# Kernel optimization log

Hardware: AMD Instinct MI355X
Metric: run time of the kernel (lower is better)

Reference implementation:

```python
import jax, jax.numpy as jnp
import numpy as np

B, C, H, W = 4, 256, 64, 64
C8 = C // 8


def setup_inputs() -> dict:
    key = jax.random.key(0)
    k1, k2, k3, k4 = jax.random.split(key, 4)
    x = jax.random.normal(k1, (B, C, H, W), dtype=jnp.float32)
    # conv1d(ks=1, bias=False) projections -> plain [out, in] matrices
    Wq = jax.random.normal(k2, (C8, C), dtype=jnp.float32) * (1.0 / np.sqrt(C))
    Wk = jax.random.normal(k3, (C8, C), dtype=jnp.float32) * (1.0 / np.sqrt(C))
    Wv = jax.random.normal(k4, (C, C), dtype=jnp.float32) * (1.0 / np.sqrt(C))
    gamma = jnp.zeros((1,), dtype=jnp.float32)
    return {"x": x, "Wq": Wq, "Wk": Wk, "Wv": Wv, "gamma": gamma}


def reference(x, Wq, Wk, Wv, gamma):
    b, c, h, w = x.shape
    xf = x.reshape(b, c, h * w)                      # [B, C, N]
    f = jnp.einsum('oc,bcn->bon', Wq, xf)            # [B, C/8, N] query
    g = jnp.einsum('oc,bcn->bon', Wk, xf)            # [B, C/8, N] key
    hv = jnp.einsum('oc,bcn->bon', Wv, xf)           # [B, C,   N] value
    # scores[b,i,j] = sum_c f[b,c,i] * g[b,c,j]; softmax over dim=1 (i)
    scores = jnp.einsum('bci,bcj->bij', f, g)        # [B, N, N]
    beta = jax.nn.softmax(scores, axis=1)
    # o[b,c,j] = sum_i hv[b,c,i] * beta[b,i,j]
    o = jnp.einsum('bci,bij->bcj', hv, beta)         # [B, C, N]
    out = gamma[0] * o + xf
    return out.reshape(b, c, h, w)
```

## Files before the change

### kernel.cpp

```cpp
#include <hip/hip_runtime.h>

#define B_  4
#define C_  256
#define C8_ 32
#define N_  4096
#define HVS_ (N_ + 64)

#define TJ 128
#define KI 64
#define SPLITS 4

typedef __attribute__((ext_vector_type(8)))  short bf16x8;
typedef __attribute__((ext_vector_type(16))) float f32x16;

union FragAB { bf16x8 v; unsigned short u[8]; };

__device__ __forceinline__ unsigned short f2bf(float x) {
    unsigned u = __float_as_uint(x);
    unsigned r = u + 0x7FFFu + ((u >> 16) & 1u);
    return (unsigned short)(r >> 16);
}
__device__ __forceinline__ unsigned pack2bf(float a, float b) {
    return (unsigned)f2bf(a) | ((unsigned)f2bf(b) << 16);
}
__device__ __forceinline__ unsigned cvtpk(float lo, float hi) {
    unsigned r;
    asm("v_cvt_pk_bf16_f32 %0, %1, %2" : "=v"(r) : "v"(lo), "v"(hi));
    return r;
}

__global__ __launch_bounds__(256) void prep_w_kernel(
    const float* __restrict__ Wq, const float* __restrict__ Wk,
    const float* __restrict__ Wv, unsigned short* __restrict__ Wbf)
{
    int idx = (blockIdx.x * 256 + threadIdx.x) * 4;
    int row = idx >> 8;
    int col = idx & 255;
    const float* src; int r;
    if (row < 32)      { src = Wq; r = row;      }
    else if (row < 64) { src = Wk; r = row - 32; }
    else               { src = Wv; r = row - 64; }
    float4 v = *(const float4*)&src[r * 256 + col];
    uint2 o; o.x = pack2bf(v.x, v.y); o.y = pack2bf(v.z, v.w);
    *(uint2*)&Wbf[idx] = o;
}

__global__ __launch_bounds__(256) void prep_x_kernel(
    const float* __restrict__ x, unsigned short* __restrict__ xT)
{
    __shared__ unsigned short T[64][66];
    int t  = threadIdx.x;
    int b  = blockIdx.z;
    int c0 = blockIdx.y * 64;
    int n0 = blockIdx.x * 64;
    const float* xb = x + (size_t)b * C_ * N_;
    int n_l = t & 63, c_l = t >> 6;
#pragma unroll
    for (int q = 0; q < 16; ++q) {
        int c = c_l * 16 + q;
        T[n_l][c] = f2bf(xb[(size_t)(c0 + c) * N_ + n0 + n_l]);
    }
    __syncthreads();
    unsigned short* xTb = xT + (size_t)b * N_ * C_;
    int c4 = (t & 15) * 4;
    int nbase = t >> 4;
#pragma unroll
    for (int q = 0; q < 4; ++q) {
        int n = nbase + 16 * q;
        uint2 u;
        u.x = (unsigned)T[n][c4]     | ((unsigned)T[n][c4 + 1] << 16);
        u.y = (unsigned)T[n][c4 + 2] | ((unsigned)T[n][c4 + 3] << 16);
        *(uint2*)&xTb[(size_t)(n0 + n) * C_ + c0 + c4] = u;
    }
}

__global__ __launch_bounds__(256) void proj_mfma_kernel(
    const unsigned short* __restrict__ Wbf, const unsigned short* __restrict__ xT,
    unsigned short* __restrict__ fT, unsigned* __restrict__ gdw,
    unsigned short* __restrict__ hv)
{
    int t = threadIdx.x, w = t >> 6, lane = t & 63;
    int half = lane >> 5, l31 = lane & 31;
    int b  = blockIdx.y;
    int n0 = blockIdx.x * 32;

    const unsigned short* xb = xT + ((size_t)b * N_ + n0 + l31) * C_;
    int nm = (w < 2) ? 3 : 2;
    int mt0 = w, mt1 = w + 4, mt2 = w + 8;

    bf16x8 bfr[16];
#pragma unroll
    for (int ks = 0; ks < 16; ++ks)
        bfr[ks] = *(const bf16x8*)&xb[ks * 16 + half * 8];

    f32x16 acc[3];
#pragma unroll
    for (int a = 0; a < 3; ++a) acc[a] = (f32x16)0.f;

#pragma unroll
    for (int ks = 0; ks < 16; ++ks) {
        int kofs = ks * 16 + half * 8;
        bf16x8 a0 = *(const bf16x8*)&Wbf[(size_t)(mt0 * 32 + l31) * 256 + kofs];
        acc[0] = __builtin_amdgcn_mfma_f32_32x32x16_bf16(a0, bfr[ks], acc[0], 0, 0, 0);
        bf16x8 a1 = *(const bf16x8*)&Wbf[(size_t)(mt1 * 32 + l31) * 256 + kofs];
        acc[1] = __builtin_amdgcn_mfma_f32_32x32x16_bf16(a1, bfr[ks], acc[1], 0, 0, 0);
        if (nm == 3) {
            bf16x8 a2 = *(const bf16x8*)&Wbf[(size_t)(mt2 * 32 + l31) * 256 + kofs];
            acc[2] = __builtin_amdgcn_mfma_f32_32x32x16_bf16(a2, bfr[ks], acc[2], 0, 0, 0);
        }
    }

    unsigned short* fTb = fT  + (size_t)b * N_ * C8_;
    unsigned*       gb  = gdw + (size_t)b * (C8_ / 2) * N_;
    unsigned short* hb  = hv  + (size_t)b * C_ * HVS_;
#pragma unroll
    for (int im = 0; im < 3; ++im) {
        if (im >= nm) break;
        int mt = (im == 0) ? mt0 : (im == 1) ? mt1 : mt2;
        if (mt == 0) {
#pragma unroll
            for (int rp = 0; rp < 8; ++rp) {
                int r = 2 * rp;
                int R = (r & 3) + 8 * (r >> 2) + 4 * half;
                *(unsigned*)&fTb[(size_t)(n0 + l31) * C8_ + R] = cvtpk(acc[0][r], acc[0][r + 1]);
            }
        } else if (mt == 1) {
#pragma unroll
            for (int rp = 0; rp < 8; ++rp) {
                int r = 2 * rp;
                int R = (r & 3) + 8 * (r >> 2) + 4 * half;
                gb[(size_t)(R >> 1) * N_ + n0 + l31] = cvtpk(acc[1][r], acc[1][r + 1]);
            }
        } else {
#pragma unroll
            for (int rp = 0; rp < 8; ++rp) {
                int r = 2 * rp;
                int R = mt * 32 + (r & 3) + 8 * (r >> 2) + 4 * half - 64;
                unsigned u = cvtpk(acc[im][r], acc[im][r + 1]);
                hb[(size_t)R * HVS_ + n0 + l31]       = (unsigned short)(u & 0xffffu);
                hb[(size_t)(R + 1) * HVS_ + n0 + l31] = (unsigned short)(u >> 16);
            }
        }
    }
}

__global__ __launch_bounds__(256, 2) void flash_kernel(
    const unsigned short* __restrict__ fT, const unsigned* __restrict__ gdw,
    const unsigned short* __restrict__ hv, unsigned* __restrict__ o_part,
    float* __restrict__ l_part)
{
    __shared__ unsigned short fS[64][40];
    __shared__ unsigned short hvT[256][72];
    __shared__ unsigned short pT[128][72];

    int t    = threadIdx.x;
    int w    = t >> 6;
    int lane = t & 63;
    int half = lane >> 5;
    int l31  = lane & 31;

    int d  = blockIdx.x;
    int jb = (d >> 3) & 31;
    int p  = (d & 7) | (((d >> 8) & 1) << 3);
    int b  = p & 3;
    int s  = p >> 2;
    int j0 = jb * TJ;

    const unsigned short* fb = fT  + (size_t)b * N_ * C8_;
    const unsigned*       gb = gdw + (size_t)b * (C8_ / 2) * N_;
    const unsigned short* hb = hv  + (size_t)b * C_ * HVS_;

    FragAB gf[2];
#pragma unroll
    for (int ks = 0; ks < 2; ++ks)
#pragma unroll
        for (int q = 0; q < 4; ++q) {
            unsigned dv = gb[(size_t)(ks * 8 + half * 4 + q) * N_ + j0 + w * 32 + l31];
            gf[ks].u[2 * q]     = (unsigned short)(dv & 0xffffu);
            gf[ks].u[2 * q + 1] = (unsigned short)(dv >> 16);
        }

    f32x16 acc[8];
#pragma unroll
    for (int a = 0; a < 8; ++a) acc[a] = (f32x16)0.f;
    float lacc = 0.f;

    int i_begin = s * (N_ / SPLITS);
    int i_end   = i_begin + N_ / SPLITS;

    for (int i0 = i_begin; i0 < i_end; i0 += KI) {
        __syncthreads();

        {
            int il = t >> 2, c4 = (t & 3) * 8;
            *(uint4*)&fS[il][c4] = *(const uint4*)&fb[(size_t)(i0 + il) * C8_ + c4];
        }
        {
            int crow  = t >> 3;
            int chunk = t & 7;
#pragma unroll
            for (int q = 0; q < 8; ++q) {
                int c = crow + 32 * q;
                *(uint4*)&hvT[c][chunk * 8] =
                    *(const uint4*)&hb[(size_t)c * HVS_ + i0 + chunk * 8];
            }
        }
        __syncthreads();

#pragma unroll
        for (int it = 0; it < 2; ++it) {
            bf16x8 af0 = *(const bf16x8*)&fS[it * 32 + l31][half * 8];
            bf16x8 af1 = *(const bf16x8*)&fS[it * 32 + l31][16 + half * 8];
            f32x16 sacc = (f32x16)0.f;
            sacc = __builtin_amdgcn_mfma_f32_32x32x16_bf16(af0, gf[0].v, sacc, 0, 0, 0);
            sacc = __builtin_amdgcn_mfma_f32_32x32x16_bf16(af1, gf[1].v, sacc, 0, 0, 0);
            float pv[16];
#pragma unroll
            for (int r = 0; r < 16; ++r) pv[r] = __expf(sacc[r]);
            float s0 = (pv[0]  + pv[1])  + (pv[2]  + pv[3]);
            float s1 = (pv[4]  + pv[5])  + (pv[6]  + pv[7]);
            float s2 = (pv[8]  + pv[9])  + (pv[10] + pv[11]);
            float s3 = (pv[12] + pv[13]) + (pv[14] + pv[15]);
            lacc += (s0 + s1) + (s2 + s3);
            int jr = w * 32 + l31;
#pragma unroll
            for (int a = 0; a < 4; ++a) {
                uint2 u;
                u.x = cvtpk(pv[4 * a + 0], pv[4 * a + 1]);
                u.y = cvtpk(pv[4 * a + 2], pv[4 * a + 3]);
                *(uint2*)&pT[jr][it * 32 + 8 * a + 4 * half] = u;
            }
        }
        __syncthreads();

        __builtin_amdgcn_s_setprio(1);
#pragma unroll
        for (int ks4 = 0; ks4 < 4; ++ks4) {
            int kofs = ks4 * 16 + half * 8;
            bf16x8 af[2], bfr[4];
#pragma unroll
            for (int ct = 0; ct < 2; ++ct)
                af[ct] = *(const bf16x8*)&hvT[w * 64 + ct * 32 + l31][kofs];
#pragma unroll
            for (int jt = 0; jt < 4; ++jt)
                bfr[jt] = *(const bf16x8*)&pT[jt * 32 + l31][kofs];
#pragma unroll
            for (int ct = 0; ct < 2; ++ct)
#pragma unroll
                for (int jt = 0; jt < 4; ++jt)
                    acc[ct * 4 + jt] = __builtin_amdgcn_mfma_f32_32x32x16_bf16(
                        af[ct], bfr[jt], acc[ct * 4 + jt], 0, 0, 0);
        }
        __builtin_amdgcn_s_setprio(0);
    }

    unsigned* ob = o_part + (size_t)(b * SPLITS + s) * (C_ / 2) * N_;
#pragma unroll
    for (int ct = 0; ct < 2; ++ct)
#pragma unroll
        for (int jt = 0; jt < 4; ++jt) {
            f32x16 a = acc[ct * 4 + jt];
#pragma unroll
            for (int rp = 0; rp < 8; ++rp) {
                int r = 2 * rp;
                unsigned u = cvtpk(a[r], a[r + 1]);
                int c = w * 64 + ct * 32 + (r & 3) + 8 * (r >> 2) + 4 * half;
                ob[(size_t)(c >> 1) * N_ + j0 + jt * 32 + l31] = u;
            }
        }
    float lsum = lacc + __shfl_down(lacc, 32);
    if (lane < 32)
        l_part[(size_t)(b * SPLITS + s) * N_ + j0 + w * 32 + lane] = lsum;
}

__global__ __launch_bounds__(256) void combine_kernel(
    const unsigned* __restrict__ o_part, const float* __restrict__ l_part,
    const float* __restrict__ x, const float* __restrict__ gamma,
    float* __restrict__ out)
{
    int j = (blockIdx.x * 256 + threadIdx.x) * 4;
    int b = blockIdx.z;
    float4 l4 = {0.f, 0.f, 0.f, 0.f};
#pragma unroll
    for (int s = 0; s < SPLITS; ++s) {
        float4 lv = *(const float4*)&l_part[(size_t)(b * SPLITS + s) * N_ + j];
        l4.x += lv.x; l4.y += lv.y; l4.z += lv.z; l4.w += lv.w;
    }
    float4 inv = {1.f / l4.x, 1.f / l4.y, 1.f / l4.z, 1.f / l4.w};
    float gm = gamma[0];
#pragma unroll
    for (int cc = 0; cc < 2; ++cc) {
        int c2 = blockIdx.y * 2 + cc;
        float4 olo = {0.f, 0.f, 0.f, 0.f}, ohi = {0.f, 0.f, 0.f, 0.f};
#pragma unroll
        for (int s = 0; s < SPLITS; ++s) {
            uint4 u = *(const uint4*)&o_part[((size_t)(b * SPLITS + s) * (C_ / 2) + c2) * N_ + j];
            olo.x += __uint_as_float(u.x << 16); ohi.x += __uint_as_float(u.x & 0xffff0000u);
            olo.y += __uint_as_float(u.y << 16); ohi.y += __uint_as_float(u.y & 0xffff0000u);
            olo.z += __uint_as_float(u.z << 16); ohi.z += __uint_as_float(u.z & 0xffff0000u);
            olo.w += __uint_as_float(u.w << 16); ohi.w += __uint_as_float(u.w & 0xffff0000u);
        }
        size_t i0 = ((size_t)b * C_ + 2 * c2) * N_ + j;
        float4 x0 = *(const float4*)&x[i0];
        float4 x1 = *(const float4*)&x[i0 + N_];
        float4 r0 = {gm * olo.x * inv.x + x0.x, gm * olo.y * inv.y + x0.y,
                     gm * olo.z * inv.z + x0.z, gm * olo.w * inv.w + x0.w};
        float4 r1 = {gm * ohi.x * inv.x + x1.x, gm * ohi.y * inv.y + x1.y,
                     gm * ohi.z * inv.z + x1.z, gm * ohi.w * inv.w + x1.w};
        *(float4*)&out[i0] = r0;
        *(float4*)&out[i0 + N_] = r1;
    }
}

extern "C" void kernel_launch(void* const* d_in, const int* in_sizes, int n_in,
                              void* d_out, int out_size, void* d_ws, size_t ws_size,
                              hipStream_t stream) {
    const float* x     = (const float*)d_in[0];
    const float* Wq    = (const float*)d_in[1];
    const float* Wk    = (const float*)d_in[2];
    const float* Wv    = (const float*)d_in[3];
    const float* gamma = (const float*)d_in[4];
    float* out = (float*)d_out;

    char* ws = (char*)d_ws;
    unsigned* o_part = (unsigned*)ws;
    float* l_part = (float*)(o_part + (size_t)SPLITS * B_ * (C_ / 2) * N_);
    unsigned short* fT  = (unsigned short*)(l_part + (size_t)SPLITS * B_ * N_);
    unsigned*       gdw = (unsigned*)(fT + (size_t)B_ * N_ * C8_);
    unsigned short* hv  = (unsigned short*)(gdw + (size_t)B_ * (C8_ / 2) * N_);
    unsigned short* Wbf = hv  + (size_t)B_ * C_ * HVS_;
    unsigned short* xT  = Wbf + (size_t)(C_ + 2 * C8_) * C_;

    prep_w_kernel<<<dim3(80), 256, 0, stream>>>(Wq, Wk, Wv, Wbf);
    prep_x_kernel<<<dim3(N_ / 64, C_ / 64, B_), 256, 0, stream>>>(x, xT);

    proj_mfma_kernel<<<dim3(N_ / 32, B_), 256, 0, stream>>>(Wbf, xT, fT, gdw, hv);

    flash_kernel<<<dim3((N_ / TJ) * B_ * SPLITS), 256, 0, stream>>>(fT, gdw, hv, o_part, l_part);

    combine_kernel<<<dim3(N_ / 1024, C_ / 4, B_), 256, 0, stream>>>(o_part, l_part, x, gamma, out);
}
```

Baseline: 146.5 us.

## Load f and hv fragments directly from global, double-buffer swizzled pT

The flash kernel no longer stages f and hv tiles through shared memory. Each wave loads its MFMA operand fragments straight into registers with inline global_load_dwordx4 and uses manual vmcnt waits so hv loads overlap the score/exp phase. The probability tile pT is double-buffered with an XOR swizzle, which cuts the loop to one barrier per iteration and avoids LDS bank conflicts. In exchange each wave loads its own fragments with less coalescing, register pressure rises, and correctness depends on the hand-placed waitcnt and barrier ordering.

```diff
diff --git a/kernel.cpp b/kernel.cpp
--- a/kernel.cpp
+++ b/kernel.cpp
@@ -26,6 +26,11 @@
 __device__ __forceinline__ unsigned cvtpk(float lo, float hi) {
     unsigned r;
     asm("v_cvt_pk_bf16_f32 %0, %1, %2" : "=v"(r) : "v"(lo), "v"(hi));
+    return r;
+}
+__device__ __forceinline__ bf16x8 gload16(const unsigned short* p) {
+    bf16x8 r;
+    asm volatile("global_load_dwordx4 %0, %1, off" : "=v"(r) : "v"(p));
     return r;
 }
 
@@ -149,9 +154,7 @@
     const unsigned short* __restrict__ hv, unsigned* __restrict__ o_part,
     float* __restrict__ l_part)
 {
-    __shared__ unsigned short fS[64][40];
-    __shared__ unsigned short hvT[256][72];
-    __shared__ unsigned short pT[128][72];
+    __shared__ unsigned short pT[2][128 * 64];
 
     int t    = threadIdx.x;
     int w    = t >> 6;
@@ -186,70 +189,77 @@
     float lacc = 0.f;
 
     int i_begin = s * (N_ / SPLITS);
-    int i_end   = i_begin + N_ / SPLITS;
-
-    for (int i0 = i_begin; i0 < i_end; i0 += KI) {
-        __syncthreads();
+
+    const unsigned short* fp  = fb + (size_t)(i_begin + l31) * C8_ + half * 8;
+    const unsigned short* hp0 = hb + (size_t)(w * 64 + l31) * HVS_ + i_begin + half * 8;
+    const unsigned short* hp1 = hp0 + (size_t)32 * HVS_;
+
+    int jr   = w * 32 + l31;
+    int rswz = l31 & 7;
+
+    for (int kit = 0; kit < (N_ / SPLITS) / KI; ++kit) {
+        bf16x8 f00 = gload16(fp);
+        bf16x8 f01 = gload16(fp + 16);
+        bf16x8 f10 = gload16(fp + 1024);
+        bf16x8 f11 = gload16(fp + 1040);
+        bf16x8 h0[4], h1[4];
+#pragma unroll
+        for (int ks4 = 0; ks4 < 4; ++ks4) h0[ks4] = gload16(hp0 + ks4 * 16);
+#pragma unroll
+        for (int ks4 = 0; ks4 < 4; ++ks4) h1[ks4] = gload16(hp1 + ks4 * 16);
+        fp  += KI * C8_;
+        hp0 += KI;
+        hp1 += KI;
+
+        char* pTc = (char*)pT[kit & 1];
+
+        asm volatile("s_waitcnt vmcnt(8)" ::: "memory");
+        __builtin_amdgcn_sched_barrier(0);
 
         {
-            int il = t >> 2, c4 = (t & 3) * 8;
-            *(uint4*)&fS[il][c4] = *(const uint4*)&fb[(size_t)(i0 + il) * C8_ + c4];
-        }
-        {
-            int crow  = t >> 3;
-            int chunk = t & 7;
-#pragma unroll
-            for (int q = 0; q < 8; ++q) {
-                int c = crow + 32 * q;
-                *(uint4*)&hvT[c][chunk * 8] =
-                    *(const uint4*)&hb[(size_t)c * HVS_ + i0 + chunk * 8];
-            }
-        }
-        __syncthreads();
-
-#pragma unroll
-        for (int it = 0; it < 2; ++it) {
-            bf16x8 af0 = *(const bf16x8*)&fS[it * 32 + l31][half * 8];
-            bf16x8 af1 = *(const bf16x8*)&fS[it * 32 + l31][16 + half * 8];
-            f32x16 sacc = (f32x16)0.f;
-            sacc = __builtin_amdgcn_mfma_f32_32x32x16_bf16(af0, gf[0].v, sacc, 0, 0, 0);
-            sacc = __builtin_amdgcn_mfma_f32_32x32x16_bf16(af1, gf[1].v, sacc, 0, 0, 0);
-            float pv[16];
-#pragma unroll
-            for (int r = 0; r < 16; ++r) pv[r] = __expf(sacc[r]);
-            float s0 = (pv[0]  + pv[1])  + (pv[2]  + pv[3]);
-            float s1 = (pv[4]  + pv[5])  + (pv[6]  + pv[7]);
-            float s2 = (pv[8]  + pv[9])  + (pv[10] + pv[11]);
-            float s3 = (pv[12] + pv[13]) + (pv[14] + pv[15]);
-            lacc += (s0 + s1) + (s2 + s3);
-            int jr = w * 32 + l31;
-#pragma unroll
-            for (int a = 0; a < 4; ++a) {
-                uint2 u;
-                u.x = cvtpk(pv[4 * a + 0], pv[4 * a + 1]);
-                u.y = cvtpk(pv[4 * a + 2], pv[4 * a + 3]);
-                *(uint2*)&pT[jr][it * 32 + 8 * a + 4 * half] = u;
-            }
-        }
-        __syncthreads();
+            bf16x8 fa[2][2] = {{f00, f01}, {f10, f11}};
+#pragma unroll
+            for (int it = 0; it < 2; ++it) {
+                f32x16 sacc = (f32x16)0.f;
+                sacc = __builtin_amdgcn_mfma_f32_32x32x16_bf16(fa[it][0], gf[0].v, sacc, 0, 0, 0);
+                sacc = __builtin_amdgcn_mfma_f32_32x32x16_bf16(fa[it][1], gf[1].v, sacc, 0, 0, 0);
+                float pv[16];
+#pragma unroll
+                for (int r = 0; r < 16; ++r) pv[r] = __expf(sacc[r]);
+                float s0 = (pv[0]  + pv[1])  + (pv[2]  + pv[3]);
+                float s1 = (pv[4]  + pv[5])  + (pv[6]  + pv[7]);
+                float s2 = (pv[8]  + pv[9])  + (pv[10] + pv[11]);
+                float s3 = (pv[12] + pv[13]) + (pv[14] + pv[15]);
+                lacc += (s0 + s1) + (s2 + s3);
+#pragma unroll
+                for (int a = 0; a < 4; ++a) {
+                    uint2 u;
+                    u.x = cvtpk(pv[4 * a + 0], pv[4 * a + 1]);
+                    u.y = cvtpk(pv[4 * a + 2], pv[4 * a + 3]);
+                    int slot = it * 4 + a;
+                    *(uint2*)(pTc + jr * 128 + (((slot ^ (jr & 7)) << 4) + (half << 3))) = u;
+                }
+            }
+        }
+
+        asm volatile("s_waitcnt lgkmcnt(0)" ::: "memory");
+        __builtin_amdgcn_s_barrier();
+        asm volatile("s_waitcnt vmcnt(0)" ::: "memory");
+        __builtin_amdgcn_sched_barrier(0);
 
         __builtin_amdgcn_s_setprio(1);
 #pragma unroll
         for (int ks4 = 0; ks4 < 4; ++ks4) {
-            int kofs = ks4 * 16 + half * 8;
-            bf16x8 af[2], bfr[4];
-#pragma unroll
-            for (int ct = 0; ct < 2; ++ct)
-                af[ct] = *(const bf16x8*)&hvT[w * 64 + ct * 32 + l31][kofs];
+            int slot = ks4 * 2 + half;
+            bf16x8 bfr[4];
 #pragma unroll
             for (int jt = 0; jt < 4; ++jt)
-                bfr[jt] = *(const bf16x8*)&pT[jt * 32 + l31][kofs];
-#pragma unroll
-            for (int ct = 0; ct < 2; ++ct)
-#pragma unroll
-                for (int jt = 0; jt < 4; ++jt)
-                    acc[ct * 4 + jt] = __builtin_amdgcn_mfma_f32_32x32x16_bf16(
-                        af[ct], bfr[jt], acc[ct * 4 + jt], 0, 0, 0);
+                bfr[jt] = *(const bf16x8*)(pTc + (jt * 32 + l31) * 128 + ((slot ^ rswz) << 4));
+#pragma unroll
+            for (int jt = 0; jt < 4; ++jt) {
+                acc[jt]     = __builtin_amdgcn_mfma_f32_32x32x16_bf16(h0[ks4], bfr[jt], acc[jt], 0, 0, 0);
+                acc[4 + jt] = __builtin_amdgcn_mfma_f32_32x32x16_bf16(h1[ks4], bfr[jt], acc[4 + jt], 0, 0, 0);
+            }
         }
         __builtin_amdgcn_s_setprio(0);
     }
```

After: 147.8 us. About the same (+0.9%).
